# Optimization experiments

Measured on AMD Instinct MI355X. Metric: run time of the kernel, lower is better.

Reference implementation:

```python
import jax, jax.numpy as jnp
import numpy as np

N_NODES = 50000
N_EDGES = 800000
NFEAT, NHID, NCLASS = 512, 256, 64


def _glorot(key, fan_in, fan_out):
    # mimics kipf-style uniform init: U(-1/sqrt(fan_out), 1/sqrt(fan_out))
    stdv = 1.0 / np.sqrt(fan_out)
    return jax.random.uniform(key, (fan_in, fan_out), jnp.float32, -stdv, stdv)


def setup_inputs() -> dict:
    key = jax.random.key(0)
    ks = jax.random.split(key, 8)
    x = jax.random.normal(ks[0], (N_NODES, NFEAT), jnp.float32)
    edge_src = jax.random.randint(ks[1], (N_EDGES,), 0, N_NODES, jnp.int32)
    edge_dst = jax.random.randint(ks[2], (N_EDGES,), 0, N_NODES, jnp.int32)
    edge_weight = jax.random.uniform(ks[3], (N_EDGES,), jnp.float32)
    W1 = _glorot(ks[4], NFEAT, NHID)
    b1 = jax.random.uniform(ks[5], (NHID,), jnp.float32, -1.0 / np.sqrt(NHID), 1.0 / np.sqrt(NHID))
    W2 = _glorot(ks[6], NHID, NCLASS)
    b2 = jax.random.uniform(ks[7], (NCLASS,), jnp.float32, -1.0 / np.sqrt(NCLASS), 1.0 / np.sqrt(NCLASS))
    return {"x": x, "W1": W1, "b1": b1, "W2": W2, "b2": b2,
            "edge_weight": edge_weight, "edge_src": edge_src, "edge_dst": edge_dst}


def _spmm(edge_src, edge_dst, edge_weight, support):
    # adj @ support with adj given as COO edge list: out[d] += w * support[s]
    msgs = support[edge_src] * edge_weight[:, None]  # [E, F]
    return jax.ops.segment_sum(msgs, edge_dst, num_segments=N_NODES)


def reference(x, W1, b1, W2, b2, edge_weight, edge_src, edge_dst):
    # layer 1: GraphConvolution -> ReLU (dropout identity in eval mode)
    h = _spmm(edge_src, edge_dst, edge_weight, x @ W1) + b1
    h = jax.nn.relu(h)
    # layer 2: GraphConvolution -> log_softmax over classes
    logits = _spmm(edge_src, edge_dst, edge_weight, h @ W2) + b2
    return jax.nn.log_softmax(logits, axis=1)
```

## Files before the change

### kernel.cpp

```cpp
#include <hip/hip_runtime.h>
#include <cstdint>


typedef unsigned short u16;
typedef unsigned int u32;
typedef unsigned long long u64;
typedef __attribute__((ext_vector_type(8))) short bf16x8;
typedef __attribute__((ext_vector_type(4))) float f32x4;

#define N_NODES 50000
#define N_EDGES 800000
#define NFEAT 512
#define NHID 256
#define NCLASS 64
#define CSTRIDE 64

#define NBUCK 196
#define BCAP 5120
#define SCB 391
#define GB1 782
#define PW1B 512
#define PW2B 64
#define FNB 3125

__device__ __forceinline__ float bf2f(u16 h) {
    union { u32 u; float f; } c; c.u = ((u32)h) << 16; return c.f;
}
__device__ __forceinline__ u16 f2bf(float f) {
    union { float f; u32 u; } c; c.f = f;
    u32 u = c.u;
    return (u16)((u + 0x7fffu + ((u >> 16) & 1u)) >> 16);
}
__device__ __forceinline__ u32 pk2(float a, float b) {
    return (u32)f2bf(a) | ((u32)f2bf(b) << 16);
}

__device__ __forceinline__ void async16(const void* g, void* l) {
    __builtin_amdgcn_global_load_lds(
        (const __attribute__((address_space(1))) void*)(uintptr_t)g,
        (__attribute__((address_space(3))) void*)(uintptr_t)l, 16, 0, 0);
}


__global__ __launch_bounds__(256) void prep0_kernel(
    const float* __restrict__ W1, u16* __restrict__ W1T,
    const float* __restrict__ W2, u16* __restrict__ W2T,
    int* __restrict__ fill) {
    int b = blockIdx.x;
    if (b < PW1B) {
        int idx = b * 256 + threadIdx.x;
        int n = idx >> 9, k = idx & 511;
        W1T[idx] = f2bf(W1[(size_t)k * NHID + n]);
    } else if (b < PW1B + PW2B) {
        int idx = (b - PW1B) * 256 + threadIdx.x;
        int n = idx >> 8, k = idx & 255;
        W2T[idx] = f2bf(W2[(size_t)k * NCLASS + n]);
    } else {
        if (threadIdx.x < NBUCK) fill[threadIdx.x] = 0;
    }
}


template <int MT, int NT, int WCOLS, int K, bool ACVT>
__device__ __forceinline__ void gemm_body(const void* __restrict__ Av,
                                          const u16* __restrict__ BT,
                                          u16* __restrict__ C, int M,
                                          int bid, u16* lds) {
    constexpr int WROWS = 4 / WCOLS;
    constexpr int RT = MT / (16 * WROWS);
    constexpr int CT = NT / (16 * WCOLS);
    u16* As = lds;
    u16* Bs = lds + MT * 64;

    const int tid  = threadIdx.x;
    const int wv   = tid >> 6, lane = tid & 63;
    const int lm   = lane & 15, quad = lane >> 4;
    const int wrow = wv / WCOLS, wcol = wv % WCOLS;
    const int m0   = bid * MT;
    const int co0 = ((0 * 4 + quad) ^ (lm & 7)) * 8;
    const int co1 = ((1 * 4 + quad) ^ (lm & 7)) * 8;

    f32x4 acc[RT][CT];
    #pragma unroll
    for (int r = 0; r < RT; ++r)
        #pragma unroll
        for (int c = 0; c < CT; ++c) acc[r][c] = (f32x4){0.f, 0.f, 0.f, 0.f};

    for (int k0 = 0; k0 < K; k0 += 64) {
        if constexpr (ACVT) {
            static_assert(MT == 64, "ACVT staging assumes MT==64 (16 elems/thread)");
            const float* Af = (const float*)Av;
            int row = tid >> 2, ko = (tid & 3) * 16;
            int gr = m0 + row; if (gr > M - 1) gr = M - 1;
            const float4* gp = (const float4*)(Af + (size_t)gr * K + k0 + ko);
            float4 f0 = gp[0], f1 = gp[1], f2 = gp[2], f3 = gp[3];
            #pragma unroll
            for (int i = 0; i < NT / 32; ++i) {
                int c = i * 256 + tid;
                int n = c >> 3, kb = c & 7;
                async16(BT + (size_t)n * K + k0 + ((kb ^ (n & 7)) * 8), Bs + c * 8);
            }
            u32 p[8] = {pk2(f0.x, f0.y), pk2(f0.z, f0.w), pk2(f1.x, f1.y), pk2(f1.z, f1.w),
                        pk2(f2.x, f2.y), pk2(f2.z, f2.w), pk2(f3.x, f3.y), pk2(f3.z, f3.w)};
            int ch0 = (2 * (tid & 3))     ^ (row & 7);
            int ch1 = (2 * (tid & 3) + 1) ^ (row & 7);
            *(int4*)(As + row * 64 + ch0 * 8) = *(int4*)&p[0];
            *(int4*)(As + row * 64 + ch1 * 8) = *(int4*)&p[4];
        } else {
            const u16* A = (const u16*)Av;
            #pragma unroll
            for (int i = 0; i < NT / 32; ++i) {
                int c = i * 256 + tid;
                int n = c >> 3, kb = c & 7;
                async16(BT + (size_t)n * K + k0 + ((kb ^ (n & 7)) * 8), Bs + c * 8);
            }
            #pragma unroll
            for (int i = 0; i < MT / 32; ++i) {
                int c = i * 256 + tid;
                int row = c >> 3, kb = c & 7;
                int gr = m0 + row; if (gr > M - 1) gr = M - 1;
                async16(A + (size_t)gr * K + k0 + ((kb ^ (row & 7)) * 8), As + c * 8);
            }
        }
        __syncthreads();

        #pragma unroll
        for (int kk = 0; kk < 2; ++kk) {
            const int co = kk ? co1 : co0;
            bf16x8 af[RT], bfv[CT];
            #pragma unroll
            for (int rt = 0; rt < RT; ++rt) {
                int row = wrow * (RT * 16) + rt * 16 + lm;
                af[rt] = *(const bf16x8*)(As + row * 64 + co);
            }
            #pragma unroll
            for (int ct = 0; ct < CT; ++ct) {
                int n = wcol * CT * 16 + ct * 16 + lm;
                bfv[ct] = *(const bf16x8*)(Bs + n * 64 + co);
            }
            #pragma unroll
            for (int rt = 0; rt < RT; ++rt)
                #pragma unroll
                for (int ct = 0; ct < CT; ++ct)
                    acc[rt][ct] = __builtin_amdgcn_mfma_f32_16x16x32_bf16(
                        af[rt], bfv[ct], acc[rt][ct], 0, 0, 0);
        }
        __syncthreads();
    }

    #pragma unroll
    for (int rt = 0; rt < RT; ++rt)
        #pragma unroll
        for (int ct = 0; ct < CT; ++ct) {
            int col = wcol * CT * 16 + ct * 16 + lm;
            #pragma unroll
            for (int r = 0; r < 4; ++r) {
                int row = wrow * (RT * 16) + rt * 16 + quad * 4 + r;
                lds[row * NT + col] = f2bf(acc[rt][ct][r]);
            }
        }
    __syncthreads();
    constexpr int NC = MT * NT / 2048;
    #pragma unroll
    for (int i = 0; i < NC; ++i) {
        int c = i * 256 + tid;
        int row = (c * 8) / NT;
        if (m0 + row < M)
            *(int4*)(C + (size_t)m0 * NT + c * 8) = *(const int4*)(lds + c * 8);
    }
}


__global__ __launch_bounds__(256) void gemm1_scatter_kernel(
    const float* __restrict__ x, const u16* __restrict__ W1T, u16* __restrict__ S1,
    const int* __restrict__ esrc, const int* __restrict__ edst,
    const float* __restrict__ ew, int* __restrict__ fill, u64* __restrict__ region) {
    __shared__ __align__(16) u16 lds[(64 + 256) * 64];
    int b = blockIdx.x;
    int tid = threadIdx.x;
    if (b < SCB) {
        int* cnt  = (int*)lds;
        int* base = cnt + NBUCK;
        if (tid < NBUCK) cnt[tid] = 0;
        __syncthreads();
        int e0 = b * 2048 + tid * 8;
        int d[8], s[8], rk[8];
        float w[8];
        bool act = (e0 < N_EDGES);
        if (act) {
            int4 d0 = *(const int4*)(edst + e0),  d1 = *(const int4*)(edst + e0 + 4);
            int4 s0 = *(const int4*)(esrc + e0),  s1 = *(const int4*)(esrc + e0 + 4);
            float4 w0 = *(const float4*)(ew + e0), w1 = *(const float4*)(ew + e0 + 4);
            d[0]=d0.x; d[1]=d0.y; d[2]=d0.z; d[3]=d0.w;
            d[4]=d1.x; d[5]=d1.y; d[6]=d1.z; d[7]=d1.w;
            s[0]=s0.x; s[1]=s0.y; s[2]=s0.z; s[3]=s0.w;
            s[4]=s1.x; s[5]=s1.y; s[6]=s1.z; s[7]=s1.w;
            w[0]=w0.x; w[1]=w0.y; w[2]=w0.z; w[3]=w0.w;
            w[4]=w1.x; w[5]=w1.y; w[6]=w1.z; w[7]=w1.w;
            #pragma unroll
            for (int i = 0; i < 8; ++i)
                rk[i] = atomicAdd(&cnt[d[i] >> 8], 1);
        }
        __syncthreads();
        if (tid < NBUCK) base[tid] = atomicAdd(&fill[tid], cnt[tid]);
        __syncthreads();
        if (act) {
            #pragma unroll
            for (int i = 0; i < 8; ++i) {
                int g = d[i] >> 8;
                int pos = base[g] + rk[i];
                if (pos < BCAP) {
                    u64 en = ((u64)(d[i] & 255) << 32) |
                             (u64)((u32)s[i] | ((u32)f2bf(w[i]) << 16));
                    region[(size_t)g * BCAP + pos] = en;
                }
            }
        }
    } else {
        gemm_body<64, 256, 4, NFEAT, true>(x, W1T, S1, N_NODES, b - SCB, lds);
    }
}


__global__ __launch_bounds__(256) void csr_sort_kernel(
    const u64* __restrict__ region, const int* __restrict__ fill,
    u32* __restrict__ csr, int* __restrict__ deg) {
    __shared__ int cnt2[256];
    int b = blockIdx.x, tid = threadIdx.x;
    cnt2[tid] = 0;
    __syncthreads();
    int Eb = fill[b]; if (Eb > BCAP) Eb = BCAP;
    for (int i = tid; i < Eb; i += 256) {
        u64 en = region[(size_t)b * BCAP + i];
        int dlo = (int)(en >> 32) & 255;
        int r = atomicAdd(&cnt2[dlo], 1);
        if (r < CSTRIDE)
            csr[(size_t)(b * 256 + dlo) * CSTRIDE + r] = (u32)en;
    }
    __syncthreads();
    int node = b * 256 + tid;
    if (node < N_NODES) {
        int dg = cnt2[tid]; if (dg > CSTRIDE) dg = CSTRIDE;
        deg[node] = dg;
    }
}


__global__ __launch_bounds__(256) void spmm1_gemm2_kernel(
    const u16* __restrict__ S, const int* __restrict__ deg,
    const u32* __restrict__ csr, const float* __restrict__ bias1,
    const u16* __restrict__ W2T, u16* __restrict__ S2) {
    __shared__ __align__(16) u16 Hs[16 * 256];
    __shared__ __align__(16) u16 Bs[64 * 64];

    const int tid  = threadIdx.x;
    const int wv   = tid >> 6, lane = tid & 63;
    const int lm   = lane & 15, quad = lane >> 4;
    const int b    = blockIdx.x;

    float4 bv = *(const float4*)(bias1 + lane * 4);

    #pragma unroll
    for (int it = 0; it < 4; ++it) {
        int lrow = wv * 4 + it;
        int node = __builtin_amdgcn_readfirstlane(b * 16 + lrow);
        int beg = node * CSTRIDE;
        int end = beg + deg[node];
        float a0 = 0.f, a1 = 0.f, a2 = 0.f, a3 = 0.f;
        int j = beg;
        for (; j + 8 <= end; j += 8) {
            u32 e[8];
            #pragma unroll
            for (int i = 0; i < 8; ++i) e[i] = csr[j + i];
            ushort4 v[8];
            #pragma unroll
            for (int i = 0; i < 8; ++i)
                v[i] = *(const ushort4*)(S + (size_t)(e[i] & 0xFFFFu) * NHID + lane * 4);
            #pragma unroll
            for (int i = 0; i < 8; ++i) {
                float w = bf2f((u16)(e[i] >> 16));
                a0 += w * bf2f(v[i].x); a1 += w * bf2f(v[i].y);
                a2 += w * bf2f(v[i].z); a3 += w * bf2f(v[i].w);
            }
        }
        for (; j < end; ++j) {
            u32 e0 = csr[j];
            float w = bf2f((u16)(e0 >> 16));
            ushort4 v0 = *(const ushort4*)(S + (size_t)(e0 & 0xFFFFu) * NHID + lane * 4);
            a0 += w * bf2f(v0.x); a1 += w * bf2f(v0.y);
            a2 += w * bf2f(v0.z); a3 += w * bf2f(v0.w);
        }
        a0 = fmaxf(a0 + bv.x, 0.f);
        a1 = fmaxf(a1 + bv.y, 0.f);
        a2 = fmaxf(a2 + bv.z, 0.f);
        a3 = fmaxf(a3 + bv.w, 0.f);
        int ch = (lane >> 1) ^ (lrow & 7);
        u32* dp = (u32*)(Hs + lrow * 256 + ch * 8 + (lane & 1) * 4);
        dp[0] = pk2(a0, a1);
        dp[1] = pk2(a2, a3);
    }
    __syncthreads();

    f32x4 acc = (f32x4){0.f, 0.f, 0.f, 0.f};
    for (int k0 = 0; k0 < NHID; k0 += 64) {
        #pragma unroll
        for (int i = 0; i < 2; ++i) {
            int c = i * 256 + tid;
            int n = c >> 3, kb = c & 7;
            async16(W2T + (size_t)n * NHID + k0 + ((kb ^ (n & 7)) * 8), Bs + c * 8);
        }
        __syncthreads();
        #pragma unroll
        for (int kk = 0; kk < 2; ++kk) {
            int ca = ((k0 >> 3) + kk * 4 + quad) ^ (lm & 7);
            bf16x8 af = *(const bf16x8*)(Hs + lm * 256 + ca * 8);
            int n = wv * 16 + lm;
            int cb = (kk * 4 + quad) ^ (n & 7);
            bf16x8 bf = *(const bf16x8*)(Bs + n * 64 + cb * 8);
            acc = __builtin_amdgcn_mfma_f32_16x16x32_bf16(af, bf, acc, 0, 0, 0);
        }
        __syncthreads();
    }

    #pragma unroll
    for (int r = 0; r < 4; ++r) {
        int row = quad * 4 + r;
        Hs[row * 64 + wv * 16 + lm] = f2bf(acc[r]);
    }
    __syncthreads();
    *(ushort4*)(S2 + (size_t)b * 1024 + tid * 4) = *(const ushort4*)(Hs + tid * 4);
}


__global__ __launch_bounds__(256) void spmm_bias_lsm_kernel(
    const u16* __restrict__ S, const int* __restrict__ deg,
    const u32* __restrict__ csr, const float* __restrict__ bias,
    float* __restrict__ out, int n) {
    int node = blockIdx.x * 4 + (threadIdx.x >> 6);
    if (node >= n) return;
    node = __builtin_amdgcn_readfirstlane(node);
    int lane = threadIdx.x & 63;
    int beg = node * CSTRIDE;
    int end = beg + deg[node];
    float acc = 0.f;
    int j = beg;
    for (; j + 8 <= end; j += 8) {
        u32 e[8];
        #pragma unroll
        for (int i = 0; i < 8; ++i) e[i] = csr[j + i];
        u16 v[8];
        #pragma unroll
        for (int i = 0; i < 8; ++i)
            v[i] = S[(size_t)(e[i] & 0xFFFFu) * NCLASS + lane];
        #pragma unroll
        for (int i = 0; i < 8; ++i)
            acc += bf2f((u16)(e[i] >> 16)) * bf2f(v[i]);
    }
    for (; j < end; ++j) {
        u32 e0 = csr[j];
        acc += bf2f((u16)(e0 >> 16)) * bf2f(S[(size_t)(e0 & 0xFFFFu) * NCLASS + lane]);
    }

    float x = acc + bias[lane];
    float m = x;
    #pragma unroll
    for (int off = 32; off > 0; off >>= 1) m = fmaxf(m, __shfl_xor(m, off));
    float e = expf(x - m);
    float ssum = e;
    #pragma unroll
    for (int off = 32; off > 0; off >>= 1) ssum += __shfl_xor(ssum, off);
    out[(size_t)node * NCLASS + lane] = x - m - logf(ssum);
}


extern "C" void kernel_launch(void* const* d_in, const int* in_sizes, int n_in,
                              void* d_out, int out_size, void* d_ws, size_t ws_size,
                              hipStream_t stream) {
    const float* x  = (const float*)d_in[0];
    const float* W1 = (const float*)d_in[1];
    const float* b1 = (const float*)d_in[2];
    const float* W2 = (const float*)d_in[3];
    const float* b2 = (const float*)d_in[4];
    const float* ew = (const float*)d_in[5];
    const int* esrc = (const int*)d_in[6];
    const int* edst = (const int*)d_in[7];
    float* out = (float*)d_out;

    char* ws = (char*)d_ws;
    size_t off = 0;
    auto take = [&](size_t bytes) -> void* {
        off = (off + 255) & ~(size_t)255;
        void* p = ws + off;
        off += bytes;
        return p;
    };
    u16* S1   = (u16*)take((size_t)N_NODES * NHID * 2);
    u16* S2   = (u16*)take((size_t)N_NODES * NCLASS * 2);
    u16* W1T  = (u16*)take((size_t)NHID * NFEAT * 2);
    u16* W2T  = (u16*)take((size_t)NCLASS * NHID * 2);
    int* deg  = (int*)take((size_t)N_NODES * 4);
    u32* csr  = (u32*)take((size_t)N_NODES * CSTRIDE * 4);
    int* fill = (int*)take((size_t)NBUCK * 4);
    u64* region = (u64*)take((size_t)NBUCK * BCAP * 8);
    (void)ws_size; (void)in_sizes; (void)n_in; (void)out_size;

    prep0_kernel<<<PW1B + PW2B + 1, 256, 0, stream>>>(W1, W1T, W2, W2T, fill);
    gemm1_scatter_kernel<<<SCB + GB1, 256, 0, stream>>>(x, W1T, S1, esrc, edst, ew,
                                                        fill, region);
    csr_sort_kernel<<<NBUCK, 256, 0, stream>>>(region, fill, csr, deg);
    spmm1_gemm2_kernel<<<FNB, 256, 0, stream>>>(S1, deg, csr, b1, W2T, S2);
    spmm_bias_lsm_kernel<<<(N_NODES + 3) / 4, 256, 0, stream>>>(
        S2, deg, csr, b2, out, N_NODES);
}
```

Measured before the change: 288.9 us.

## Double-buffer GEMM1 A tiles, read weights directly from global, unroll SpMM gathers

Replaces the generic GEMM body with a specialised GEMM1 that double-buffers the converted x tile in LDS, prefetching the next K-chunk while the MFMAs run. B fragments are read straight from global/L2 instead of being staged in LDS, which shrinks LDS use so more blocks can be resident. The fused SpMM+GEMM2 kernel likewise reads W2T directly, and both SpMM kernels gain a 16-wide gather unroll for more memory-level parallelism. A standalone gemm2_kernel is added but does not appear to be launched here. Uncoalesced direct global B reads and higher register pressure from the wider unrolls could offset the gains.

New measurement: 302.5 us. +4.7%, slower.

```diff
diff --git a/kernel.cpp b/kernel.cpp
--- a/kernel.cpp
+++ b/kernel.cpp
@@ -19,6 +19,7 @@
 #define BCAP 5120
 #define SCB 391
 #define GB1 782
+#define GB2 391
 #define PW1B 512
 #define PW2B 64
 #define FNB 3125
@@ -61,112 +62,98 @@
 }
 
 
-template <int MT, int NT, int WCOLS, int K, bool ACVT>
-__device__ __forceinline__ void gemm_body(const void* __restrict__ Av,
-                                          const u16* __restrict__ BT,
-                                          u16* __restrict__ C, int M,
-                                          int bid, u16* lds) {
-    constexpr int WROWS = 4 / WCOLS;
-    constexpr int RT = MT / (16 * WROWS);
-    constexpr int CT = NT / (16 * WCOLS);
-    u16* As = lds;
-    u16* Bs = lds + MT * 64;
-
-    const int tid  = threadIdx.x;
-    const int wv   = tid >> 6, lane = tid & 63;
-    const int lm   = lane & 15, quad = lane >> 4;
-    const int wrow = wv / WCOLS, wcol = wv % WCOLS;
-    const int m0   = bid * MT;
+__device__ __forceinline__ void gemm1_body(const float* __restrict__ x,
+                                           const u16* __restrict__ BT,
+                                           u16* __restrict__ C, int M,
+                                           int bid, u16* lds) {
+    const int tid = threadIdx.x;
+    const int wcol = tid >> 6, lane = tid & 63;
+    const int lm = lane & 15, quad = lane >> 4;
+    const int m0 = bid * 64;
     const int co0 = ((0 * 4 + quad) ^ (lm & 7)) * 8;
     const int co1 = ((1 * 4 + quad) ^ (lm & 7)) * 8;
-
-    f32x4 acc[RT][CT];
-    #pragma unroll
-    for (int r = 0; r < RT; ++r)
-        #pragma unroll
-        for (int c = 0; c < CT; ++c) acc[r][c] = (f32x4){0.f, 0.f, 0.f, 0.f};
-
-    for (int k0 = 0; k0 < K; k0 += 64) {
-        if constexpr (ACVT) {
-            static_assert(MT == 64, "ACVT staging assumes MT==64 (16 elems/thread)");
-            const float* Af = (const float*)Av;
-            int row = tid >> 2, ko = (tid & 3) * 16;
-            int gr = m0 + row; if (gr > M - 1) gr = M - 1;
-            const float4* gp = (const float4*)(Af + (size_t)gr * K + k0 + ko);
-            float4 f0 = gp[0], f1 = gp[1], f2 = gp[2], f3 = gp[3];
-            #pragma unroll
-            for (int i = 0; i < NT / 32; ++i) {
-                int c = i * 256 + tid;
-                int n = c >> 3, kb = c & 7;
-                async16(BT + (size_t)n * K + k0 + ((kb ^ (n & 7)) * 8), Bs + c * 8);
+    const int arow = tid >> 2;
+    int gr = m0 + arow; if (gr > M - 1) gr = M - 1;
+    const float* gpb = x + (size_t)gr * NFEAT + (tid & 3) * 16;
+    const int ch0 = (2 * (tid & 3)) ^ (arow & 7);
+    const int ch1 = (2 * (tid & 3) + 1) ^ (arow & 7);
+
+    f32x4 acc[4][4];
+    #pragma unroll
+    for (int r = 0; r < 4; ++r)
+        #pragma unroll
+        for (int c = 0; c < 4; ++c) acc[r][c] = (f32x4){0.f, 0.f, 0.f, 0.f};
+
+    {
+        const float4* gp = (const float4*)gpb;
+        float4 f0 = gp[0], f1 = gp[1], f2 = gp[2], f3 = gp[3];
+        u32 p[8] = {pk2(f0.x, f0.y), pk2(f0.z, f0.w), pk2(f1.x, f1.y), pk2(f1.z, f1.w),
+                    pk2(f2.x, f2.y), pk2(f2.z, f2.w), pk2(f3.x, f3.y), pk2(f3.z, f3.w)};
+        *(int4*)(lds + arow * 64 + ch0 * 8) = *(int4*)&p[0];
+        *(int4*)(lds + arow * 64 + ch1 * 8) = *(int4*)&p[4];
+    }
+    __syncthreads();
+
+    for (int t = 0; t < 8; ++t) {
+        u16* As = lds + (t & 1) * 4096;
+        u16* An = lds + ((t + 1) & 1) * 4096;
+        bool pf = (t + 1) < 8;
+        float4 f0, f1, f2, f3;
+        if (pf) {
+            const float4* gp = (const float4*)(gpb + (t + 1) * 64);
+            f0 = gp[0]; f1 = gp[1]; f2 = gp[2]; f3 = gp[3];
+        }
+        #pragma unroll
+        for (int kk = 0; kk < 2; ++kk) {
+            const int co = kk ? co1 : co0;
+            bf16x8 af[4], bfv[4];
+            #pragma unroll
+            for (int rt = 0; rt < 4; ++rt)
+                af[rt] = *(const bf16x8*)(As + (rt * 16 + lm) * 64 + co);
+            #pragma unroll
+            for (int ct = 0; ct < 4; ++ct) {
+                int n = wcol * 64 + ct * 16 + lm;
+                bfv[ct] = *(const bf16x8*)(BT + (size_t)n * NFEAT + t * 64 + kk * 32 + quad * 8);
             }
+            #pragma unroll
+            for (int rt = 0; rt < 4; ++rt)
+                #pragma unroll
+                for (int ct = 0; ct < 4; ++ct)
+                    acc[rt][ct] = __builtin_amdgcn_mfma_f32_16x16x32_bf16(
+                        af[rt], bfv[ct], acc[rt][ct], 0, 0, 0);
+        }
+        if (pf) {
             u32 p[8] = {pk2(f0.x, f0.y), pk2(f0.z, f0.w), pk2(f1.x, f1.y), pk2(f1.z, f1.w),
                         pk2(f2.x, f2.y), pk2(f2.z, f2.w), pk2(f3.x, f3.y), pk2(f3.z, f3.w)};
-            int ch0 = (2 * (tid & 3))     ^ (row & 7);
-            int ch1 = (2 * (tid & 3) + 1) ^ (row & 7);
-            *(int4*)(As + row * 64 + ch0 * 8) = *(int4*)&p[0];
-            *(int4*)(As + row * 64 + ch1 * 8) = *(int4*)&p[4];
-        } else {
-            const u16* A = (const u16*)Av;
-            #pragma unroll
-            for (int i = 0; i < NT / 32; ++i) {
-                int c = i * 256 + tid;
-                int n = c >> 3, kb = c & 7;
-                async16(BT + (size_t)n * K + k0 + ((kb ^ (n & 7)) * 8), Bs + c * 8);
-            }
-            #pragma unroll
-            for (int i = 0; i < MT / 32; ++i) {
-                int c = i * 256 + tid;
-                int row = c >> 3, kb = c & 7;
-                int gr = m0 + row; if (gr > M - 1) gr = M - 1;
-                async16(A + (size_t)gr * K + k0 + ((kb ^ (row & 7)) * 8), As + c * 8);
-            }
-        }
-        __syncthreads();
-
-        #pragma unroll
-        for (int kk = 0; kk < 2; ++kk) {
-            const int co = kk ? co1 : co0;
-            bf16x8 af[RT], bfv[CT];
-            #pragma unroll
-            for (int rt = 0; rt < RT; ++rt) {
-                int row = wrow * (RT * 16) + rt * 16 + lm;
-                af[rt] = *(const bf16x8*)(As + row * 64 + co);
-            }
-            #pragma unroll
-            for (int ct = 0; ct < CT; ++ct) {
-                int n = wcol * CT * 16 + ct * 16 + lm;
-                bfv[ct] = *(const bf16x8*)(Bs + n * 64 + co);
-            }
-            #pragma unroll
-            for (int rt = 0; rt < RT; ++rt)
+            *(int4*)(An + arow * 64 + ch0 * 8) = *(int4*)&p[0];
+            *(int4*)(An + arow * 64 + ch1 * 8) = *(int4*)&p[4];
+        }
+        __syncthreads();
+    }
+
+    #pragma unroll
+    for (int h = 0; h < 2; ++h) {
+        if ((wcol >> 1) == h) {
+            #pragma unroll
+            for (int rt = 0; rt < 4; ++rt)
                 #pragma unroll
-                for (int ct = 0; ct < CT; ++ct)
-                    acc[rt][ct] = __builtin_amdgcn_mfma_f32_16x16x32_bf16(
-                        af[rt], bfv[ct], acc[rt][ct], 0, 0, 0);
-        }
-        __syncthreads();
-    }
-
-    #pragma unroll
-    for (int rt = 0; rt < RT; ++rt)
-        #pragma unroll
-        for (int ct = 0; ct < CT; ++ct) {
-            int col = wcol * CT * 16 + ct * 16 + lm;
-            #pragma unroll
-            for (int r = 0; r < 4; ++r) {
-                int row = wrow * (RT * 16) + rt * 16 + quad * 4 + r;
-                lds[row * NT + col] = f2bf(acc[rt][ct][r]);
-            }
-        }
-    __syncthreads();
-    constexpr int NC = MT * NT / 2048;
-    #pragma unroll
-    for (int i = 0; i < NC; ++i) {
-        int c = i * 256 + tid;
-        int row = (c * 8) / NT;
-        if (m0 + row < M)
-            *(int4*)(C + (size_t)m0 * NT + c * 8) = *(const int4*)(lds + c * 8);
+                for (int ct = 0; ct < 4; ++ct) {
+                    int col = wcol * 64 + ct * 16 + lm - h * 128;
+                    #pragma unroll
+                    for (int r = 0; r < 4; ++r)
+                        lds[(rt * 16 + quad * 4 + r) * 128 + col] = f2bf(acc[rt][ct][r]);
+                }
+        }
+        __syncthreads();
+        #pragma unroll
+        for (int i = 0; i < 4; ++i) {
+            int c = i * 256 + tid;
+            int row = c >> 4, c8 = c & 15;
+            if (m0 + row < M)
+                *(int4*)(C + (size_t)(m0 + row) * 256 + h * 128 + c8 * 8) =
+                    *(const int4*)(lds + c * 8);
+        }
+        __syncthreads();
     }
 }
 
@@ -175,7 +162,7 @@
     const float* __restrict__ x, const u16* __restrict__ W1T, u16* __restrict__ S1,
     const int* __restrict__ esrc, const int* __restrict__ edst,
     const float* __restrict__ ew, int* __restrict__ fill, u64* __restrict__ region) {
-    __shared__ __align__(16) u16 lds[(64 + 256) * 64];
+    __shared__ __align__(16) u16 lds[8192];
     int b = blockIdx.x;
     int tid = threadIdx.x;
     if (b < SCB) {
@@ -217,7 +204,83 @@
             }
         }
     } else {
-        gemm_body<64, 256, 4, NFEAT, true>(x, W1T, S1, N_NODES, b - SCB, lds);
+        gemm1_body(x, W1T, S1, N_NODES, b - SCB, lds);
+    }
+}
+
+
+__global__ __launch_bounds__(256) void gemm2_kernel(const u16* __restrict__ H,
+                                                    const u16* __restrict__ W2T,
+                                                    u16* __restrict__ S2, int M) {
+    __shared__ __align__(16) u16 lds[16384];
+    const int tid = threadIdx.x;
+    const int wv = tid >> 6, lane = tid & 63;
+    const int wrow = wv >> 1, wcol = wv & 1;
+    const int lm = lane & 15, quad = lane >> 4;
+    const int m0 = blockIdx.x * 128;
+    const int co0 = ((0 * 4 + quad) ^ (lm & 7)) * 8;
+    const int co1 = ((1 * 4 + quad) ^ (lm & 7)) * 8;
+
+    f32x4 acc[4][2];
+    #pragma unroll
+    for (int r = 0; r < 4; ++r)
+        #pragma unroll
+        for (int c = 0; c < 2; ++c) acc[r][c] = (f32x4){0.f, 0.f, 0.f, 0.f};
+
+    auto stage = [&](u16* dst, int t) {
+        #pragma unroll
+        for (int i = 0; i < 4; ++i) {
+            int c = i * 256 + tid;
+            int row = c >> 3, kb = c & 7;
+            int gr = m0 + row; if (gr > M - 1) gr = M - 1;
+            async16(H + (size_t)gr * NHID + t * 64 + ((kb ^ (row & 7)) * 8), dst + c * 8);
+        }
+    };
+
+    stage(lds, 0);
+    __syncthreads();
+
+    for (int t = 0; t < 4; ++t) {
+        u16* As = lds + (t & 1) * 8192;
+        if (t + 1 < 4) stage(lds + ((t + 1) & 1) * 8192, t + 1);
+        #pragma unroll
+        for (int kk = 0; kk < 2; ++kk) {
+            const int co = kk ? co1 : co0;
+            bf16x8 af[4], bfv[2];
+            #pragma unroll
+            for (int rt = 0; rt < 4; ++rt)
+                af[rt] = *(const bf16x8*)(As + (wrow * 64 + rt * 16 + lm) * 64 + co);
+            #pragma unroll
+            for (int ct = 0; ct < 2; ++ct) {
+                int n = wcol * 32 + ct * 16 + lm;
+                bfv[ct] = *(const bf16x8*)(W2T + (size_t)n * NHID + t * 64 + kk * 32 + quad * 8);
+            }
+            #pragma unroll
+            for (int rt = 0; rt < 4; ++rt)
+                #pragma unroll
+                for (int ct = 0; ct < 2; ++ct)
+                    acc[rt][ct] = __builtin_amdgcn_mfma_f32_16x16x32_bf16(
+                        af[rt], bfv[ct], acc[rt][ct], 0, 0, 0);
+        }
+        __syncthreads();
+    }
+
+    #pragma unroll
+    for (int rt = 0; rt < 4; ++rt)
+        #pragma unroll
+        for (int ct = 0; ct < 2; ++ct) {
+            int col = wcol * 32 + ct * 16 + lm;
+            #pragma unroll
+            for (int r = 0; r < 4; ++r)
+                lds[(wrow * 64 + rt * 16 + quad * 4 + r) * 64 + col] = f2bf(acc[rt][ct][r]);
+        }
+    __syncthreads();
+    #pragma unroll
+    for (int i = 0; i < 4; ++i) {
+        int c = i * 256 + tid;
+        int row = c >> 3;
+        if (m0 + row < M)
+            *(int4*)(S2 + (size_t)m0 * 64 + c * 8) = *(const int4*)(lds + c * 8);
     }
 }
 
@@ -251,7 +314,6 @@
     const u32* __restrict__ csr, const float* __restrict__ bias1,
     const u16* __restrict__ W2T, u16* __restrict__ S2) {
     __shared__ __align__(16) u16 Hs[16 * 256];
-    __shared__ __align__(16) u16 Bs[64 * 64];
 
     const int tid  = threadIdx.x;
     const int wv   = tid >> 6, lane = tid & 63;
@@ -268,6 +330,21 @@
         int end = beg + deg[node];
         float a0 = 0.f, a1 = 0.f, a2 = 0.f, a3 = 0.f;
         int j = beg;
+        for (; j + 16 <= end; j += 16) {
+            u32 e[16];
+            #pragma unroll
+            for (int i = 0; i < 16; ++i) e[i] = csr[j + i];
+            ushort4 v[16];
+            #pragma unroll
+            for (int i = 0; i < 16; ++i)
+                v[i] = *(const ushort4*)(S + (size_t)(e[i] & 0xFFFFu) * NHID + lane * 4);
+            #pragma unroll
+            for (int i = 0; i < 16; ++i) {
+                float w = bf2f((u16)(e[i] >> 16));
+                a0 += w * bf2f(v[i].x); a1 += w * bf2f(v[i].y);
+                a2 += w * bf2f(v[i].z); a3 += w * bf2f(v[i].w);
+            }
+        }
         for (; j + 8 <= end; j += 8) {
             u32 e[8];
             #pragma unroll
@@ -302,25 +379,18 @@
     __syncthreads();
 
     f32x4 acc = (f32x4){0.f, 0.f, 0.f, 0.f};
+    #pragma unroll
     for (int k0 = 0; k0 < NHID; k0 += 64) {
-        #pragma unroll
-        for (int i = 0; i < 2; ++i) {
-            int c = i * 256 + tid;
-            int n = c >> 3, kb = c & 7;
-            async16(W2T + (size_t)n * NHID + k0 + ((kb ^ (n & 7)) * 8), Bs + c * 8);
-        }
-        __syncthreads();
         #pragma unroll
         for (int kk = 0; kk < 2; ++kk) {
             int ca = ((k0 >> 3) + kk * 4 + quad) ^ (lm & 7);
             bf16x8 af = *(const bf16x8*)(Hs + lm * 256 + ca * 8);
             int n = wv * 16 + lm;
-            int cb = (kk * 4 + quad) ^ (n & 7);
-            bf16x8 bf = *(const bf16x8*)(Bs + n * 64 + cb * 8);
+            bf16x8 bf = *(const bf16x8*)(W2T + (size_t)n * NHID + k0 + kk * 32 + quad * 8);
             acc = __builtin_amdgcn_mfma_f32_16x16x32_bf16(af, bf, acc, 0, 0, 0);
         }
-        __syncthreads();
-    }
+    }
+    __syncthreads();
 
     #pragma unroll
     for (int r = 0; r < 4; ++r) {
@@ -344,6 +414,18 @@
     int end = beg + deg[node];
     float acc = 0.f;
     int j = beg;
+    for (; j + 16 <= end; j += 16) {
+        u32 e[16];
+        #pragma unroll
+        for (int i = 0; i < 16; ++i) e[i] = csr[j + i];
+        u16 v[16];
+        #pragma unroll
+        for (int i = 0; i < 16; ++i)
+            v[i] = S[(size_t)(e[i] & 0xFFFFu) * NCLASS + lane];
+        #pragma unroll
+        for (int i = 0; i < 16; ++i)
+            acc += bf2f((u16)(e[i] >> 16)) * bf2f(v[i]);
+    }
     for (; j + 8 <= end; j += 8) {
         u32 e[8];
         #pragma unroll
```

## Regroup kernels to overlap weight prep with scatter and GEMM1 with CSR sort

Applied to the files above, without the earlier changes.

Moves the weight transpose/convert into the edge-scatter kernel and co-schedules the CSR bucket sort with the layer-1 GEMM in one launch, replacing the fill-zeroing block with a memset. This changes which independent stages share a grid, so the small prep work hides behind the scatter and the sort hides behind the GEMM. It also deepens the SpMM gather loops to 16 edges per batch for more memory-level parallelism, and reads W2T fragments straight from global memory in the fused GEMM2, dropping the LDS staging and barriers. The cost is more registers in the gather loops and uncoalesced, repeated global reads of W2T.

New measurement: 288.6 us. Within noise of the previous version (-0.1%).

```diff
diff --git a/kernel.cpp b/kernel.cpp
--- a/kernel.cpp
+++ b/kernel.cpp
@@ -42,145 +42,15 @@
 }
 
 
-__global__ __launch_bounds__(256) void prep0_kernel(
+__global__ __launch_bounds__(256) void prep_scatter_kernel(
     const float* __restrict__ W1, u16* __restrict__ W1T,
     const float* __restrict__ W2, u16* __restrict__ W2T,
-    int* __restrict__ fill) {
-    int b = blockIdx.x;
-    if (b < PW1B) {
-        int idx = b * 256 + threadIdx.x;
-        int n = idx >> 9, k = idx & 511;
-        W1T[idx] = f2bf(W1[(size_t)k * NHID + n]);
-    } else if (b < PW1B + PW2B) {
-        int idx = (b - PW1B) * 256 + threadIdx.x;
-        int n = idx >> 8, k = idx & 255;
-        W2T[idx] = f2bf(W2[(size_t)k * NCLASS + n]);
-    } else {
-        if (threadIdx.x < NBUCK) fill[threadIdx.x] = 0;
-    }
-}
-
-
-template <int MT, int NT, int WCOLS, int K, bool ACVT>
-__device__ __forceinline__ void gemm_body(const void* __restrict__ Av,
-                                          const u16* __restrict__ BT,
-                                          u16* __restrict__ C, int M,
-                                          int bid, u16* lds) {
-    constexpr int WROWS = 4 / WCOLS;
-    constexpr int RT = MT / (16 * WROWS);
-    constexpr int CT = NT / (16 * WCOLS);
-    u16* As = lds;
-    u16* Bs = lds + MT * 64;
-
-    const int tid  = threadIdx.x;
-    const int wv   = tid >> 6, lane = tid & 63;
-    const int lm   = lane & 15, quad = lane >> 4;
-    const int wrow = wv / WCOLS, wcol = wv % WCOLS;
-    const int m0   = bid * MT;
-    const int co0 = ((0 * 4 + quad) ^ (lm & 7)) * 8;
-    const int co1 = ((1 * 4 + quad) ^ (lm & 7)) * 8;
-
-    f32x4 acc[RT][CT];
-    #pragma unroll
-    for (int r = 0; r < RT; ++r)
-        #pragma unroll
-        for (int c = 0; c < CT; ++c) acc[r][c] = (f32x4){0.f, 0.f, 0.f, 0.f};
-
-    for (int k0 = 0; k0 < K; k0 += 64) {
-        if constexpr (ACVT) {
-            static_assert(MT == 64, "ACVT staging assumes MT==64 (16 elems/thread)");
-            const float* Af = (const float*)Av;
-            int row = tid >> 2, ko = (tid & 3) * 16;
-            int gr = m0 + row; if (gr > M - 1) gr = M - 1;
-            const float4* gp = (const float4*)(Af + (size_t)gr * K + k0 + ko);
-            float4 f0 = gp[0], f1 = gp[1], f2 = gp[2], f3 = gp[3];
-            #pragma unroll
-            for (int i = 0; i < NT / 32; ++i) {
-                int c = i * 256 + tid;
-                int n = c >> 3, kb = c & 7;
-                async16(BT + (size_t)n * K + k0 + ((kb ^ (n & 7)) * 8), Bs + c * 8);
-            }
-            u32 p[8] = {pk2(f0.x, f0.y), pk2(f0.z, f0.w), pk2(f1.x, f1.y), pk2(f1.z, f1.w),
-                        pk2(f2.x, f2.y), pk2(f2.z, f2.w), pk2(f3.x, f3.y), pk2(f3.z, f3.w)};
-            int ch0 = (2 * (tid & 3))     ^ (row & 7);
-            int ch1 = (2 * (tid & 3) + 1) ^ (row & 7);
-            *(int4*)(As + row * 64 + ch0 * 8) = *(int4*)&p[0];
-            *(int4*)(As + row * 64 + ch1 * 8) = *(int4*)&p[4];
-        } else {
-            const u16* A = (const u16*)Av;
-            #pragma unroll
-            for (int i = 0; i < NT / 32; ++i) {
-                int c = i * 256 + tid;
-                int n = c >> 3, kb = c & 7;
-                async16(BT + (size_t)n * K + k0 + ((kb ^ (n & 7)) * 8), Bs + c * 8);
-            }
-            #pragma unroll
-            for (int i = 0; i < MT / 32; ++i) {
-                int c = i * 256 + tid;
-                int row = c >> 3, kb = c & 7;
-                int gr = m0 + row; if (gr > M - 1) gr = M - 1;
-                async16(A + (size_t)gr * K + k0 + ((kb ^ (row & 7)) * 8), As + c * 8);
-            }
-        }
-        __syncthreads();
-
-        #pragma unroll
-        for (int kk = 0; kk < 2; ++kk) {
-            const int co = kk ? co1 : co0;
-            bf16x8 af[RT], bfv[CT];
-            #pragma unroll
-            for (int rt = 0; rt < RT; ++rt) {
-                int row = wrow * (RT * 16) + rt * 16 + lm;
-                af[rt] = *(const bf16x8*)(As + row * 64 + co);
-            }
-            #pragma unroll
-            for (int ct = 0; ct < CT; ++ct) {
-                int n = wcol * CT * 16 + ct * 16 + lm;
-                bfv[ct] = *(const bf16x8*)(Bs + n * 64 + co);
-            }
-            #pragma unroll
-            for (int rt = 0; rt < RT; ++rt)
-                #pragma unroll
-                for (int ct = 0; ct < CT; ++ct)
-                    acc[rt][ct] = __builtin_amdgcn_mfma_f32_16x16x32_bf16(
-                        af[rt], bfv[ct], acc[rt][ct], 0, 0, 0);
-        }
-        __syncthreads();
-    }
-
-    #pragma unroll
-    for (int rt = 0; rt < RT; ++rt)
-        #pragma unroll
-        for (int ct = 0; ct < CT; ++ct) {
-            int col = wcol * CT * 16 + ct * 16 + lm;
-            #pragma unroll
-            for (int r = 0; r < 4; ++r) {
-                int row = wrow * (RT * 16) + rt * 16 + quad * 4 + r;
-                lds[row * NT + col] = f2bf(acc[rt][ct][r]);
-            }
-        }
-    __syncthreads();
-    constexpr int NC = MT * NT / 2048;
-    #pragma unroll
-    for (int i = 0; i < NC; ++i) {
-        int c = i * 256 + tid;
-        int row = (c * 8) / NT;
-        if (m0 + row < M)
-            *(int4*)(C + (size_t)m0 * NT + c * 8) = *(const int4*)(lds + c * 8);
-    }
-}
-
-
-__global__ __launch_bounds__(256) void gemm1_scatter_kernel(
-    const float* __restrict__ x, const u16* __restrict__ W1T, u16* __restrict__ S1,
     const int* __restrict__ esrc, const int* __restrict__ edst,
     const float* __restrict__ ew, int* __restrict__ fill, u64* __restrict__ region) {
-    __shared__ __align__(16) u16 lds[(64 + 256) * 64];
-    int b = blockIdx.x;
-    int tid = threadIdx.x;
+    __shared__ int cnt[NBUCK];
+    __shared__ int base[NBUCK];
+    int b = blockIdx.x, tid = threadIdx.x;
     if (b < SCB) {
-        int* cnt  = (int*)lds;
-        int* base = cnt + NBUCK;
         if (tid < NBUCK) cnt[tid] = 0;
         __syncthreads();
         int e0 = b * 2048 + tid * 8;
@@ -216,32 +86,154 @@
                 }
             }
         }
+    } else if (b < SCB + PW1B) {
+        int idx = (b - SCB) * 256 + tid;
+        int n = idx >> 9, k = idx & 511;
+        W1T[idx] = f2bf(W1[(size_t)k * NHID + n]);
     } else {
-        gemm_body<64, 256, 4, NFEAT, true>(x, W1T, S1, N_NODES, b - SCB, lds);
-    }
-}
-
-
-__global__ __launch_bounds__(256) void csr_sort_kernel(
+        int idx = (b - SCB - PW1B) * 256 + tid;
+        int n = idx >> 8, k = idx & 255;
+        W2T[idx] = f2bf(W2[(size_t)k * NCLASS + n]);
+    }
+}
+
+
+template <int MT, int NT, int WCOLS, int K, bool ACVT>
+__device__ __forceinline__ void gemm_body(const void* __restrict__ Av,
+                                          const u16* __restrict__ BT,
+                                          u16* __restrict__ C, int M,
+                                          int bid, u16* lds) {
+    constexpr int WROWS = 4 / WCOLS;
+    constexpr int RT = MT / (16 * WROWS);
+    constexpr int CT = NT / (16 * WCOLS);
+    u16* As = lds;
+    u16* Bs = lds + MT * 64;
+
+    const int tid  = threadIdx.x;
+    const int wv   = tid >> 6, lane = tid & 63;
+    const int lm   = lane & 15, quad = lane >> 4;
+    const int wrow = wv / WCOLS, wcol = wv % WCOLS;
+    const int m0   = bid * MT;
+    const int co0 = ((0 * 4 + quad) ^ (lm & 7)) * 8;
+    const int co1 = ((1 * 4 + quad) ^ (lm & 7)) * 8;
+
+    f32x4 acc[RT][CT];
+    #pragma unroll
+    for (int r = 0; r < RT; ++r)
+        #pragma unroll
+        for (int c = 0; c < CT; ++c) acc[r][c] = (f32x4){0.f, 0.f, 0.f, 0.f};
+
+    for (int k0 = 0; k0 < K; k0 += 64) {
+        if constexpr (ACVT) {
+            static_assert(MT == 64, "ACVT staging assumes MT==64 (16 elems/thread)");
+            const float* Af = (const float*)Av;
+            int row = tid >> 2, ko = (tid & 3) * 16;
+            int gr = m0 + row; if (gr > M - 1) gr = M - 1;
+            const float4* gp = (const float4*)(Af + (size_t)gr * K + k0 + ko);
+            float4 f0 = gp[0], f1 = gp[1], f2 = gp[2], f3 = gp[3];
+            #pragma unroll
+            for (int i = 0; i < NT / 32; ++i) {
+                int c = i * 256 + tid;
+                int n = c >> 3, kb = c & 7;
+                async16(BT + (size_t)n * K + k0 + ((kb ^ (n & 7)) * 8), Bs + c * 8);
+            }
+            u32 p[8] = {pk2(f0.x, f0.y), pk2(f0.z, f0.w), pk2(f1.x, f1.y), pk2(f1.z, f1.w),
+                        pk2(f2.x, f2.y), pk2(f2.z, f2.w), pk2(f3.x, f3.y), pk2(f3.z, f3.w)};
+            int ch0 = (2 * (tid & 3))     ^ (row & 7);
+            int ch1 = (2 * (tid & 3) + 1) ^ (row & 7);
+            *(int4*)(As + row * 64 + ch0 * 8) = *(int4*)&p[0];
+            *(int4*)(As + row * 64 + ch1 * 8) = *(int4*)&p[4];
+        } else {
+            const u16* A = (const u16*)Av;
+            #pragma unroll
+            for (int i = 0; i < NT / 32; ++i) {
+                int c = i * 256 + tid;
+                int n = c >> 3, kb = c & 7;
+                async16(BT + (size_t)n * K + k0 + ((kb ^ (n & 7)) * 8), Bs + c * 8);
+            }
+            #pragma unroll
+            for (int i = 0; i < MT / 32; ++i) {
+                int c = i * 256 + tid;
+                int row = c >> 3, kb = c & 7;
+                int gr = m0 + row; if (gr > M - 1) gr = M - 1;
+                async16(A + (size_t)gr * K + k0 + ((kb ^ (row & 7)) * 8), As + c * 8);
+            }
+        }
+        __syncthreads();
+
+        #pragma unroll
+        for (int kk = 0; kk < 2; ++kk) {
+            const int co = kk ? co1 : co0;
+            bf16x8 af[RT], bfv[CT];
+            #pragma unroll
+            for (int rt = 0; rt < RT; ++rt) {
+                int row = wrow * (RT * 16) + rt * 16 + lm;
+                af[rt] = *(const bf16x8*)(As + row * 64 + co);
+            }
+            #pragma unroll
+            for (int ct = 0; ct < CT; ++ct) {
+                int n = wcol * CT * 16 + ct * 16 + lm;
+                bfv[ct] = *(const bf16x8*)(Bs + n * 64 + co);
+            }
+            #pragma unroll
+            for (int rt = 0; rt < RT; ++rt)
+                #pragma unroll
+                for (int ct = 0; ct < CT; ++ct)
+                    acc[rt][ct] = __builtin_amdgcn_mfma_f32_16x16x32_bf16(
+                        af[rt], bfv[ct], acc[rt][ct], 0, 0, 0);
+        }
+        __syncthreads();
+    }
+
+    #pragma unroll
+    for (int rt = 0; rt < RT; ++rt)
+        #pragma unroll
+        for (int ct = 0; ct < CT; ++ct) {
+            int col = wcol * CT * 16 + ct * 16 + lm;
+            #pragma unroll
+            for (int r = 0; r < 4; ++r) {
+                int row = wrow * (RT * 16) + rt * 16 + quad * 4 + r;
+                lds[row * NT + col] = f2bf(acc[rt][ct][r]);
+            }
+        }
+    __syncthreads();
+    constexpr int NC = MT * NT / 2048;
+    #pragma unroll
+    for (int i = 0; i < NC; ++i) {
+        int c = i * 256 + tid;
+        int row = (c * 8) / NT;
+        if (m0 + row < M)
+            *(int4*)(C + (size_t)m0 * NT + c * 8) = *(const int4*)(lds + c * 8);
+    }
+}
+
+
+__global__ __launch_bounds__(256) void gemm1_sort_kernel(
+    const float* __restrict__ x, const u16* __restrict__ W1T, u16* __restrict__ S1,
     const u64* __restrict__ region, const int* __restrict__ fill,
     u32* __restrict__ csr, int* __restrict__ deg) {
-    __shared__ int cnt2[256];
+    __shared__ __align__(16) u16 lds[(64 + 256) * 64];
     int b = blockIdx.x, tid = threadIdx.x;
-    cnt2[tid] = 0;
-    __syncthreads();
-    int Eb = fill[b]; if (Eb > BCAP) Eb = BCAP;
-    for (int i = tid; i < Eb; i += 256) {
-        u64 en = region[(size_t)b * BCAP + i];
-        int dlo = (int)(en >> 32) & 255;
-        int r = atomicAdd(&cnt2[dlo], 1);
-        if (r < CSTRIDE)
-            csr[(size_t)(b * 256 + dlo) * CSTRIDE + r] = (u32)en;
-    }
-    __syncthreads();
-    int node = b * 256 + tid;
-    if (node < N_NODES) {
-        int dg = cnt2[tid]; if (dg > CSTRIDE) dg = CSTRIDE;
-        deg[node] = dg;
+    if (b < NBUCK) {
+        int* cnt2 = (int*)lds;
+        cnt2[tid] = 0;
+        __syncthreads();
+        int Eb = fill[b]; if (Eb > BCAP) Eb = BCAP;
+        for (int i = tid; i < Eb; i += 256) {
+            u64 en = region[(size_t)b * BCAP + i];
+            int dlo = (int)(en >> 32) & 255;
+            int r = atomicAdd(&cnt2[dlo], 1);
+            if (r < CSTRIDE)
+                csr[(size_t)(b * 256 + dlo) * CSTRIDE + r] = (u32)en;
+        }
+        __syncthreads();
+        int node = b * 256 + tid;
+        if (node < N_NODES) {
+            int dg = cnt2[tid]; if (dg > CSTRIDE) dg = CSTRIDE;
+            deg[node] = dg;
+        }
+    } else {
+        gemm_body<64, 256, 4, NFEAT, true>(x, W1T, S1, N_NODES, b - NBUCK, lds);
     }
 }
 
@@ -251,7 +243,6 @@
     const u32* __restrict__ csr, const float* __restrict__ bias1,
     const u16* __restrict__ W2T, u16* __restrict__ S2) {
     __shared__ __align__(16) u16 Hs[16 * 256];
-    __shared__ __align__(16) u16 Bs[64 * 64];
 
     const int tid  = threadIdx.x;
     const int wv   = tid >> 6, lane = tid & 63;
@@ -268,6 +259,21 @@
         int end = beg + deg[node];
         float a0 = 0.f, a1 = 0.f, a2 = 0.f, a3 = 0.f;
         int j = beg;
+        for (; j + 16 <= end; j += 16) {
+            u32 e[16];
+            #pragma unroll
+            for (int i = 0; i < 16; ++i) e[i] = csr[j + i];
+            ushort4 v[16];
+            #pragma unroll
+            for (int i = 0; i < 16; ++i)
+                v[i] = *(const ushort4*)(S + (size_t)(e[i] & 0xFFFFu) * NHID + lane * 4);
+            #pragma unroll
+            for (int i = 0; i < 16; ++i) {
+                float w = bf2f((u16)(e[i] >> 16));
+                a0 += w * bf2f(v[i].x); a1 += w * bf2f(v[i].y);
+                a2 += w * bf2f(v[i].z); a3 += w * bf2f(v[i].w);
+            }
+        }
         for (; j + 8 <= end; j += 8) {
             u32 e[8];
             #pragma unroll
@@ -302,25 +308,18 @@
     __syncthreads();
 
     f32x4 acc = (f32x4){0.f, 0.f, 0.f, 0.f};
+    #pragma unroll
     for (int k0 = 0; k0 < NHID; k0 += 64) {
-        #pragma unroll
-        for (int i = 0; i < 2; ++i) {
-            int c = i * 256 + tid;
-            int n = c >> 3, kb = c & 7;
-            async16(W2T + (size_t)n * NHID + k0 + ((kb ^ (n & 7)) * 8), Bs + c * 8);
-        }
-        __syncthreads();
         #pragma unroll
         for (int kk = 0; kk < 2; ++kk) {
             int ca = ((k0 >> 3) + kk * 4 + quad) ^ (lm & 7);
             bf16x8 af = *(const bf16x8*)(Hs + lm * 256 + ca * 8);
             int n = wv * 16 + lm;
-            int cb = (kk * 4 + quad) ^ (n & 7);
-            bf16x8 bf = *(const bf16x8*)(Bs + n * 64 + cb * 8);
+            bf16x8 bf = *(const bf16x8*)(W2T + (size_t)n * NHID + k0 + kk * 32 + quad * 8);
             acc = __builtin_amdgcn_mfma_f32_16x16x32_bf16(af, bf, acc, 0, 0, 0);
         }
-        __syncthreads();
-    }
+    }
+    __syncthreads();
 
     #pragma unroll
     for (int r = 0; r < 4; ++r) {
@@ -344,6 +343,18 @@
     int end = beg + deg[node];
     float acc = 0.f;
     int j = beg;
+    for (; j + 16 <= end; j += 16) {
+        u32 e[16];
+        #pragma unroll
+        for (int i = 0; i < 16; ++i) e[i] = csr[j + i];
+        u16 v[16];
+        #pragma unroll
+        for (int i = 0; i < 16; ++i)
+            v[i] = S[(size_t)(e[i] & 0xFFFFu) * NCLASS + lane];
+        #pragma unroll
+        for (int i = 0; i < 16; ++i)
+            acc += bf2f((u16)(e[i] >> 16)) * bf2f(v[i]);
+    }
     for (; j + 8 <= end; j += 8) {
         u32 e[8];
         #pragma unroll
@@ -404,10 +415,11 @@
     u64* region = (u64*)take((size_t)NBUCK * BCAP * 8);
     (void)ws_size; (void)in_sizes; (void)n_in; (void)out_size;
 
-    prep0_kernel<<<PW1B + PW2B + 1, 256, 0, stream>>>(W1, W1T, W2, W2T, fill);
-    gemm1_scatter_kernel<<<SCB + GB1, 256, 0, stream>>>(x, W1T, S1, esrc, edst, ew,
-                                                        fill, region);
-    csr_sort_kernel<<<NBUCK, 256, 0, stream>>>(region, fill, csr, deg);
+    hipMemsetAsync(fill, 0, (size_t)NBUCK * 4, stream);
+    prep_scatter_kernel<<<SCB + PW1B + PW2B, 256, 0, stream>>>(
+        W1, W1T, W2, W2T, esrc, edst, ew, fill, region);
+    gemm1_sort_kernel<<<NBUCK + GB1, 256, 0, stream>>>(
+        x, W1T, S1, region, fill, csr, deg);
     spmm1_gemm2_kernel<<<FNB, 256, 0, stream>>>(S1, deg, csr, b1, W2T, S2);
     spmm_bias_lsm_kernel<<<(N_NODES + 3) / 4, 256, 0, stream>>>(
         S2, deg, csr, b2, out, N_NODES);
```
